# Kernel optimization log

Measured on AMD Instinct MI355X. Metric: run time of the kernel, lower is better.

## Reference

```python
import jax, jax.numpy as jnp
import numpy as np

B, T, C, H = 4, 4096, 1024, 16

def setup_inputs() -> dict:
    key = jax.random.key(0)
    k1, k2, k3, k4 = jax.random.split(key, 4)
    return {
        "x": jax.random.normal(k1, (B, T, C), dtype=jnp.float32),
        "W_attn": jax.random.normal(k2, (C, C), dtype=jnp.float32) * 0.02,
        "b_attn": jnp.zeros((C,), dtype=jnp.float32),
        "W_proj": jax.random.normal(k3, (C, C), dtype=jnp.float32) * 0.02,
        "b_proj": jnp.zeros((C,), dtype=jnp.float32),
        "temp": jnp.ones((H, 1), dtype=jnp.float32),
        "n_head": H,
    }

def reference(x, W_attn, b_attn, W_proj, b_proj, temp, n_head):
    Bb, Tt, Cc = x.shape
    D = Cc // n_head
    # c_attn (torch Linear: x @ W.T + b)
    w = x @ W_attn.T + b_attn                         # (B,T,C)
    w = w.reshape(Bb, Tt, n_head, D).transpose(0, 2, 1, 3)  # (B,H,T,D)
    # F.normalize over token axis (dim=-2), eps=1e-12
    norm = jnp.maximum(jnp.sqrt(jnp.sum(w * w, axis=-2, keepdims=True)), 1e-12)
    w_normed = w / norm
    tmp = jnp.sum(w_normed ** 2, axis=-1) * temp      # (B,H,T) * (H,1) -> (B,H,T)
    Pi = jax.nn.softmax(tmp, axis=1)                  # softmax over heads
    Pi_prob = Pi / (jnp.sum(Pi, axis=-1, keepdims=True) + 1e-8)  # (B,H,T)
    dots = jnp.einsum('bht,bhtd->bhd', Pi_prob, w ** 2)          # (B,H,D)
    attn = 1.0 / (1.0 + dots)                         # (B,H,D)
    y = -(w * Pi[..., None]) * attn[:, :, None, :]    # (B,H,T,D)
    y = y.transpose(0, 2, 1, 3).reshape(Bb, Tt, Cc)
    return y @ W_proj.T + b_proj
```

## Files before the change

kernel.cpp:

```cpp
#include <hip/hip_runtime.h>
#include <hip/hip_bf16.h>

#define BB 4
#define TT 4096
#define CC 1024
#define HH 16
#define DD 64

typedef __attribute__((ext_vector_type(8))) short short8;
typedef __attribute__((ext_vector_type(8))) __bf16 bf16x8;
typedef __attribute__((ext_vector_type(4))) float f32x4;

static __device__ __forceinline__ unsigned short f2bf(float f) {
    unsigned int u = __builtin_bit_cast(unsigned int, f);
    unsigned int r = (u + 0x7FFFu + ((u >> 16) & 1u)) >> 16;
    return (unsigned short)r;
}
static __device__ __forceinline__ float bf2f(unsigned short h) {
    return __builtin_bit_cast(float, ((unsigned int)h) << 16);
}
static __device__ __forceinline__ bf16x8 cvt8(f32x4 a, f32x4 b) {
    bf16x8 r;
    r[0] = (__bf16)a[0]; r[1] = (__bf16)a[1]; r[2] = (__bf16)a[2]; r[3] = (__bf16)a[3];
    r[4] = (__bf16)b[0]; r[5] = (__bf16)b[1]; r[6] = (__bf16)b[2]; r[7] = (__bf16)b[3];
    return r;
}

__global__ void k_f32_to_bf16(const float* __restrict__ src,
                              unsigned short* __restrict__ dst, int n4) {
    int i = blockIdx.x * 256 + threadIdx.x;
    if (i >= n4) return;
    float4 v = ((const float4*)src)[i];
    ushort4 o;
    o.x = f2bf(v.x); o.y = f2bf(v.y); o.z = f2bf(v.z); o.w = f2bf(v.w);
    ((ushort4*)dst)[i] = o;
}

#define GBM 256
#define GBN 256
#define GBK 32

static __device__ __forceinline__ void stage_b16(
    const unsigned short* __restrict__ Gbase, unsigned short* lbase,
    int k0, int K, int wave, int lane)
{
    #pragma unroll
    for (int q = 0; q < 2; ++q) {
        int c = (wave * 2 + q) * 64 + lane;
        int r = c >> 2;
        int j = c & 3;
        int srcj = (j - (r >> 1)) & 3;
        const unsigned short* g = Gbase + (size_t)r * K + k0 + srcj * 8;
        __builtin_amdgcn_global_load_lds(
            (const __attribute__((address_space(1))) void*)g,
            (__attribute__((address_space(3))) void*)(lbase + (wave * 2 + q) * 512),
            16, 0, 0);
    }
}

static __device__ __forceinline__ void stage_a_f32(
    const float* __restrict__ Gbase, float* lbase,
    int k0, int K, int wave, int lane)
{
    #pragma unroll
    for (int q = 0; q < 4; ++q) {
        int c = (wave * 4 + q) * 64 + lane;
        int r = c >> 3;
        int s = c & 7;
        int srcs = s ^ (r & 7);
        const float* g = Gbase + (size_t)r * K + k0 + srcs * 4;
        __builtin_amdgcn_global_load_lds(
            (const __attribute__((address_space(1))) void*)g,
            (__attribute__((address_space(3))) void*)(lbase + (wave * 4 + q) * 256),
            16, 0, 0);
    }
}

template<int MODE>
__global__ __launch_bounds__(512, 2)
void k_gemm256(const void* __restrict__ Asrc,
               const unsigned short* __restrict__ Bsrc,
               const float* __restrict__ bias,
               void* __restrict__ Cout,
               float* __restrict__ S,
               int M, int N, int K)
{
    __shared__ unsigned int Au[3][(MODE == 0) ? 8192 : 4096];
    __shared__ unsigned short Bl[3][8192];
    const int tid  = threadIdx.x;
    const int wave = tid >> 6;
    const int lane = tid & 63;
    const int wr = wave >> 2, wc = wave & 3;
    const int fr = lane & 15, hi = lane >> 4;

    const int wg  = blockIdx.x;
    const int swz = (wg & 7) * 32 + (wg >> 3);
    const int bn  = swz & 3;
    const int bm  = swz >> 2;
    const int nt  = K / GBK;

    const float* Afg = (const float*)Asrc + (size_t)(bm * GBM) * K;
    const unsigned short* Abg = (const unsigned short*)Asrc + (size_t)(bm * GBM) * K;
    const unsigned short* Bbase = Bsrc + (size_t)(bn * GBN) * K;

    f32x4 acc[8][4] = {};

    if (MODE == 0) stage_a_f32(Afg, (float*)Au[0], 0, K, wave, lane);
    else           stage_b16(Abg, (unsigned short*)Au[0], 0, K, wave, lane);
    stage_b16(Bbase, Bl[0], 0, K, wave, lane);
    if (MODE == 0) stage_a_f32(Afg, (float*)Au[1], GBK, K, wave, lane);
    else           stage_b16(Abg, (unsigned short*)Au[1], GBK, K, wave, lane);
    stage_b16(Bbase, Bl[1], GBK, K, wave, lane);
    if (MODE == 0) { asm volatile("s_waitcnt vmcnt(6)" ::: "memory"); }
    else           { asm volatile("s_waitcnt vmcnt(4)" ::: "memory"); }
    __builtin_amdgcn_s_barrier();

    const int sl    = (hi + (fr >> 1)) & 3;
    const int boff  = (wc * 64 + fr) * 32 + sl * 8;
    const int aoffB = (wr * 128 + fr) * 32 + sl * 8;
    const int sw0   = ((2 * hi)     ^ (fr & 7)) * 4;
    const int sw1   = ((2 * hi + 1) ^ (fr & 7)) * 4;
    const int arow  = (wr * 128 + fr) * 32;

    int rb = 0;
    for (int kt = 0; kt < nt; ++kt) {
        const int wb = (rb == 0) ? 2 : rb - 1;
        int ks = kt + 2; if (ks >= nt) ks = nt - 1;
        const unsigned short* Bc = Bl[rb];

        bf16x8 af0[4]; short8 bfr[4];
        if (MODE == 0) {
            const float* Af = (const float*)Au[rb];
            #pragma unroll
            for (int mi = 0; mi < 4; ++mi) {
                f32x4 lo = *(const f32x4*)&Af[arow + mi * 512 + sw0];
                f32x4 h4 = *(const f32x4*)&Af[arow + mi * 512 + sw1];
                af0[mi] = cvt8(lo, h4);
            }
        } else {
            const unsigned short* Ab = (const unsigned short*)Au[rb];
            #pragma unroll
            for (int mi = 0; mi < 4; ++mi)
                af0[mi] = __builtin_bit_cast(bf16x8, *(const short8*)&Ab[aoffB + mi * 512]);
        }
        #pragma unroll
        for (int ni = 0; ni < 4; ++ni)
            bfr[ni] = *(const short8*)&Bc[boff + ni * 512];
        if (MODE == 0) stage_a_f32(Afg, (float*)Au[wb], ks * GBK, K, wave, lane);
        else           stage_b16(Abg, (unsigned short*)Au[wb], ks * GBK, K, wave, lane);
        stage_b16(Bbase, Bl[wb], ks * GBK, K, wave, lane);
        __builtin_amdgcn_s_barrier();
        __builtin_amdgcn_s_setprio(1);
        #pragma unroll
        for (int mi = 0; mi < 4; ++mi)
            #pragma unroll
            for (int ni = 0; ni < 4; ++ni)
                acc[mi][ni] = __builtin_amdgcn_mfma_f32_16x16x32_bf16(
                    af0[mi], __builtin_bit_cast(bf16x8, bfr[ni]), acc[mi][ni], 0, 0, 0);
        __builtin_amdgcn_s_setprio(0);
        __builtin_amdgcn_s_barrier();

        bf16x8 af1[4];
        if (MODE == 0) {
            const float* Af = (const float*)Au[rb];
            #pragma unroll
            for (int mi = 0; mi < 4; ++mi) {
                f32x4 lo = *(const f32x4*)&Af[arow + (4 + mi) * 512 + sw0];
                f32x4 h4 = *(const f32x4*)&Af[arow + (4 + mi) * 512 + sw1];
                af1[mi] = cvt8(lo, h4);
            }
        } else {
            const unsigned short* Ab = (const unsigned short*)Au[rb];
            #pragma unroll
            for (int mi = 0; mi < 4; ++mi)
                af1[mi] = __builtin_bit_cast(bf16x8, *(const short8*)&Ab[aoffB + (4 + mi) * 512]);
        }
        if (MODE == 0) { asm volatile("s_waitcnt vmcnt(6)" ::: "memory"); }
        else           { asm volatile("s_waitcnt vmcnt(4)" ::: "memory"); }
        __builtin_amdgcn_s_barrier();
        __builtin_amdgcn_s_setprio(1);
        #pragma unroll
        for (int mi = 0; mi < 4; ++mi)
            #pragma unroll
            for (int ni = 0; ni < 4; ++ni)
                acc[4 + mi][ni] = __builtin_amdgcn_mfma_f32_16x16x32_bf16(
                    af1[mi], __builtin_bit_cast(bf16x8, bfr[ni]), acc[4 + mi][ni], 0, 0, 0);
        __builtin_amdgcn_s_setprio(0);
        __builtin_amdgcn_s_barrier();

        rb = (rb == 2) ? 0 : rb + 1;
    }

    __syncthreads();

    const int cg = fr;
    const int rg = hi * 4;
    float* sblk = (float*)&Bl[0][0];
    if (MODE == 0) {
        if (tid < GBN) sblk[tid] = 0.f;
        __syncthreads();
    }
    float csum[4] = {};
    #pragma unroll
    for (int mi = 0; mi < 8; ++mi) {
        #pragma unroll
        for (int ni = 0; ni < 4; ++ni) {
            int col = bn * GBN + wc * 64 + ni * 16 + cg;
            float bv = bias[col];
            #pragma unroll
            for (int j = 0; j < 4; ++j) {
                int row = bm * GBM + wr * 128 + mi * 16 + rg + j;
                float v = acc[mi][ni][j] + bv;
                if (MODE == 0) {
                    ((unsigned short*)Cout)[(size_t)row * N + col] = f2bf(v);
                    csum[ni] += v * v;
                } else {
                    ((float*)Cout)[(size_t)row * N + col] = v;
                }
            }
        }
    }
    if (MODE == 0) {
        #pragma unroll
        for (int ni = 0; ni < 4; ++ni)
            atomicAdd(&sblk[wc * 64 + ni * 16 + cg], csum[ni]);
        __syncthreads();
        const int b = bm >> 4;
        if (tid < GBN) atomicAdd(&S[b * CC + bn * GBN + tid], sblk[tid]);
    }
}

__global__ __launch_bounds__(256)
void k_row_softmax(const unsigned short* __restrict__ w16, const float* __restrict__ S,
                   const float* __restrict__ temp,
                   float* __restrict__ Pi, float* __restrict__ dotsU,
                   float* __restrict__ sumPi)
{
    __shared__ float dots_local[CC];
    __shared__ float sPi_local[HH];
    const int tid  = threadIdx.x;
    const int wave = tid >> 6;
    const int lane = tid & 63;
    const int bb   = blockIdx.x >> 7;
    const int tile = blockIdx.x & 127;

    for (int c = tid; c < CC; c += 256) dots_local[c] = 0.f;
    if (tid < HH) sPi_local[tid] = 0.f;
    __syncthreads();

    const int g3 = lane >> 3;
    const int li = lane & 7;

    float inv[2][8], tsc[2];
    #pragma unroll
    for (int q = 0; q < 2; ++q) {
        int c = q * 512 + lane * 8;
        const float4* sp = (const float4*)&S[bb * CC + c];
        float4 s0 = sp[0], s1 = sp[1];
        inv[q][0] = 1.f / fmaxf(s0.x, 1e-24f); inv[q][1] = 1.f / fmaxf(s0.y, 1e-24f);
        inv[q][2] = 1.f / fmaxf(s0.z, 1e-24f); inv[q][3] = 1.f / fmaxf(s0.w, 1e-24f);
        inv[q][4] = 1.f / fmaxf(s1.x, 1e-24f); inv[q][5] = 1.f / fmaxf(s1.y, 1e-24f);
        inv[q][6] = 1.f / fmaxf(s1.z, 1e-24f); inv[q][7] = 1.f / fmaxf(s1.w, 1e-24f);
        tsc[q] = temp[q * 8 + g3];
    }

    float dacc[2][8] = {};
    float sPiAcc[2] = {};

    for (int i = 0; i < 8; ++i) {
        int t = tile * 32 + wave * 8 + i;
        const unsigned short* row = w16 + ((size_t)bb * TT + t) * CC;
        float wf[2][8];
        float pq[2];
        #pragma unroll
        for (int q = 0; q < 2; ++q) {
            short8 v = *(const short8*)&row[q * 512 + lane * 8];
            float s = 0.f;
            #pragma unroll
            for (int j = 0; j < 8; ++j) {
                wf[q][j] = bf2f((unsigned short)v[j]);
                s += wf[q][j] * wf[q][j] * inv[q][j];
            }
            pq[q] = s;
        }
        #pragma unroll
        for (int off = 1; off < 8; off <<= 1) {
            pq[0] += __shfl_xor(pq[0], off);
            pq[1] += __shfl_xor(pq[1], off);
        }
        pq[0] *= tsc[0]; pq[1] *= tsc[1];
        float mx = fmaxf(pq[0], pq[1]);
        mx = fmaxf(mx, __shfl_xor(mx, 8));
        mx = fmaxf(mx, __shfl_xor(mx, 16));
        mx = fmaxf(mx, __shfl_xor(mx, 32));
        float e0 = __expf(pq[0] - mx), e1 = __expf(pq[1] - mx);
        float ss = e0 + e1;
        ss += __shfl_xor(ss, 8);
        ss += __shfl_xor(ss, 16);
        ss += __shfl_xor(ss, 32);
        float rs = 1.f / ss;
        float piv[2] = { e0 * rs, e1 * rs };
        #pragma unroll
        for (int q = 0; q < 2; ++q) {
            #pragma unroll
            for (int j = 0; j < 8; ++j)
                dacc[q][j] += piv[q] * wf[q][j] * wf[q][j];
            if (li == 0) {
                Pi[((size_t)(bb * HH + q * 8 + g3)) * TT + t] = piv[q];
                sPiAcc[q] += piv[q];
            }
        }
    }

    #pragma unroll
    for (int q = 0; q < 2; ++q) {
        int c = q * 512 + lane * 8;
        #pragma unroll
        for (int j = 0; j < 8; ++j)
            atomicAdd(&dots_local[c + j], dacc[q][j]);
        if (li == 0) atomicAdd(&sPi_local[q * 8 + g3], sPiAcc[q]);
    }
    __syncthreads();
    for (int c = tid; c < CC; c += 256) atomicAdd(&dotsU[bb * CC + c], dots_local[c]);
    if (tid < HH) atomicAdd(&sumPi[bb * HH + tid], sPi_local[tid]);
}

__global__ void k_attnscale(const float* __restrict__ dotsU,
                            const float* __restrict__ sumPi,
                            float* __restrict__ attnScale) {
    int i = blockIdx.x * 256 + threadIdx.x;
    if (i >= BB * CC) return;
    int b = i >> 10;
    int h = (i >> 6) & 15;
    float sp = sumPi[b * HH + h] + 1e-8f;
    attnScale[i] = 1.f / (1.f + dotsU[i] / sp);
}

__global__ void k_make_y(unsigned short* __restrict__ wy, const float* __restrict__ Pi,
                         const float* __restrict__ attnScale)
{
    size_t i = (size_t)blockIdx.x * 256 + threadIdx.x;
    size_t flat = i * 8;
    int c = (int)(flat & (CC - 1));
    size_t bt = flat >> 10;
    int t = (int)(bt & (TT - 1));
    int b = (int)(bt >> 12);
    int h = c >> 6;
    float pi = Pi[((size_t)(b * HH + h)) * TT + t];
    short8 wv = *(const short8*)&wy[flat];
    f32x4 a0 = *(const f32x4*)&attnScale[b * CC + c];
    f32x4 a1 = *(const f32x4*)&attnScale[b * CC + c + 4];
    short8 o;
    #pragma unroll
    for (int j = 0; j < 4; ++j) {
        o[j]     = (short)f2bf(-(bf2f((unsigned short)wv[j])     * pi) * a0[j]);
        o[4 + j] = (short)f2bf(-(bf2f((unsigned short)wv[4 + j]) * pi) * a1[j]);
    }
    *(short8*)&wy[flat] = o;
}

extern "C" void kernel_launch(void* const* d_in, const int* in_sizes, int n_in,
                              void* d_out, int out_size, void* d_ws, size_t ws_size,
                              hipStream_t stream) {
    const float* x      = (const float*)d_in[0];
    const float* W_attn = (const float*)d_in[1];
    const float* b_attn = (const float*)d_in[2];
    const float* W_proj = (const float*)d_in[3];
    const float* b_proj = (const float*)d_in[4];
    const float* temp   = (const float*)d_in[5];

    char* ws = (char*)d_ws;
    unsigned short* w16  = (unsigned short*)(ws);
    unsigned short* Wa16 = (unsigned short*)(ws + 33554432);
    unsigned short* Wp16 = (unsigned short*)(ws + 35651584);
    float* Pi        = (float*)(ws + 37748736);
    float* S         = (float*)(ws + 38797312);
    float* dotsU     = (float*)(ws + 38813696);
    float* sumPi     = (float*)(ws + 38830080);
    float* attnScale = (float*)(ws + 38830336);

    k_f32_to_bf16<<<dim3(1024), dim3(256), 0, stream>>>(W_attn, Wa16, 262144);
    k_f32_to_bf16<<<dim3(1024), dim3(256), 0, stream>>>(W_proj, Wp16, 262144);

    hipMemsetAsync(S, 0, 16384 + 16384 + 256, stream);

    k_gemm256<0><<<dim3(256), dim3(512), 0, stream>>>(
        x, Wa16, b_attn, w16, S, BB * TT, CC, CC);

    k_row_softmax<<<dim3(512), dim3(256), 0, stream>>>(w16, S, temp, Pi, dotsU, sumPi);

    k_attnscale<<<dim3(16), dim3(256), 0, stream>>>(dotsU, sumPi, attnScale);

    k_make_y<<<dim3(8192), dim3(256), 0, stream>>>(w16, Pi, attnScale);

    k_gemm256<1><<<dim3(256), dim3(512), 0, stream>>>(
        w16, Wp16, b_proj, d_out, nullptr, BB * TT, CC, CC);
}
```

Before: 150.6 us.

## Pre-convert x to bf16 and use a 4-stage unified LDS pipeline in GEMM

Adds a separate kernel that converts x from fp32 to bf16 into the output buffer as scratch, so the first GEMM loads bf16 A tiles instead of fp32 tiles that it converted in registers. The GEMM is reworked to use a single 4-deep LDS ring holding both A and B tiles, with prefetch three steps ahead. The A and B stages are split across the two half-iterations, and B fragments are reloaded in each half. This removes the per-iteration fp32 LDS traffic and conversion work, at the cost of an extra pass over x in global memory and more LDS per block.

```diff
diff --git a/kernel.cpp b/kernel.cpp
--- a/kernel.cpp
+++ b/kernel.cpp
@@ -18,12 +18,6 @@
 }
 static __device__ __forceinline__ float bf2f(unsigned short h) {
     return __builtin_bit_cast(float, ((unsigned int)h) << 16);
-}
-static __device__ __forceinline__ bf16x8 cvt8(f32x4 a, f32x4 b) {
-    bf16x8 r;
-    r[0] = (__bf16)a[0]; r[1] = (__bf16)a[1]; r[2] = (__bf16)a[2]; r[3] = (__bf16)a[3];
-    r[4] = (__bf16)b[0]; r[5] = (__bf16)b[1]; r[6] = (__bf16)b[2]; r[7] = (__bf16)b[3];
-    return r;
 }
 
 __global__ void k_f32_to_bf16(const float* __restrict__ src,
@@ -40,7 +34,7 @@
 #define GBN 256
 #define GBK 32
 
-static __device__ __forceinline__ void stage_b16(
+static __device__ __forceinline__ void stage_tile32(
     const unsigned short* __restrict__ Gbase, unsigned short* lbase,
     int k0, int K, int wave, int lane)
 {
@@ -58,144 +52,101 @@
     }
 }
 
-static __device__ __forceinline__ void stage_a_f32(
-    const float* __restrict__ Gbase, float* lbase,
-    int k0, int K, int wave, int lane)
-{
-    #pragma unroll
-    for (int q = 0; q < 4; ++q) {
-        int c = (wave * 4 + q) * 64 + lane;
-        int r = c >> 3;
-        int s = c & 7;
-        int srcs = s ^ (r & 7);
-        const float* g = Gbase + (size_t)r * K + k0 + srcs * 4;
-        __builtin_amdgcn_global_load_lds(
-            (const __attribute__((address_space(1))) void*)g,
-            (__attribute__((address_space(3))) void*)(lbase + (wave * 4 + q) * 256),
-            16, 0, 0);
-    }
-}
-
 template<int MODE>
 __global__ __launch_bounds__(512, 2)
-void k_gemm256(const void* __restrict__ Asrc,
-               const unsigned short* __restrict__ Bsrc,
+void k_gemm256(const unsigned short* __restrict__ A,
+               const unsigned short* __restrict__ B,
                const float* __restrict__ bias,
                void* __restrict__ Cout,
                float* __restrict__ S,
                int M, int N, int K)
 {
-    __shared__ unsigned int Au[3][(MODE == 0) ? 8192 : 4096];
-    __shared__ unsigned short Bl[3][8192];
+    __shared__ unsigned short lds[4][16384];
     const int tid  = threadIdx.x;
     const int wave = tid >> 6;
     const int lane = tid & 63;
-    const int wr = wave >> 2, wc = wave & 3;
-    const int fr = lane & 15, hi = lane >> 4;
+    const int wr = wave >> 2;
+    const int wc = wave & 3;
+    const int fr = lane & 15;
+    const int hi = lane >> 4;
 
     const int wg  = blockIdx.x;
     const int swz = (wg & 7) * 32 + (wg >> 3);
     const int bn  = swz & 3;
     const int bm  = swz >> 2;
-    const int nt  = K / GBK;
-
-    const float* Afg = (const float*)Asrc + (size_t)(bm * GBM) * K;
-    const unsigned short* Abg = (const unsigned short*)Asrc + (size_t)(bm * GBM) * K;
-    const unsigned short* Bbase = Bsrc + (size_t)(bn * GBN) * K;
+
+    const unsigned short* Abase = A + (size_t)(bm * GBM) * K;
+    const unsigned short* Bbase = B + (size_t)(bn * GBN) * K;
+
+    const int nt = K / GBK;
+
+    const int sl   = (hi + (fr >> 1)) & 3;
+    const int aoff = (wr * 128 + fr) * 32 + sl * 8;
+    const int boff = 8192 + (wc * 64 + fr) * 32 + sl * 8;
 
     f32x4 acc[8][4] = {};
 
-    if (MODE == 0) stage_a_f32(Afg, (float*)Au[0], 0, K, wave, lane);
-    else           stage_b16(Abg, (unsigned short*)Au[0], 0, K, wave, lane);
-    stage_b16(Bbase, Bl[0], 0, K, wave, lane);
-    if (MODE == 0) stage_a_f32(Afg, (float*)Au[1], GBK, K, wave, lane);
-    else           stage_b16(Abg, (unsigned short*)Au[1], GBK, K, wave, lane);
-    stage_b16(Bbase, Bl[1], GBK, K, wave, lane);
-    if (MODE == 0) { asm volatile("s_waitcnt vmcnt(6)" ::: "memory"); }
-    else           { asm volatile("s_waitcnt vmcnt(4)" ::: "memory"); }
+    stage_tile32(Abase, lds[0],        0,       K, wave, lane);
+    stage_tile32(Bbase, lds[0] + 8192, 0,       K, wave, lane);
+    stage_tile32(Abase, lds[1],        GBK,     K, wave, lane);
+    stage_tile32(Bbase, lds[1] + 8192, GBK,     K, wave, lane);
+    stage_tile32(Abase, lds[2],        2 * GBK, K, wave, lane);
+    stage_tile32(Bbase, lds[2] + 8192, 2 * GBK, K, wave, lane);
+    asm volatile("s_waitcnt vmcnt(8)" ::: "memory");
     __builtin_amdgcn_s_barrier();
 
-    const int sl    = (hi + (fr >> 1)) & 3;
-    const int boff  = (wc * 64 + fr) * 32 + sl * 8;
-    const int aoffB = (wr * 128 + fr) * 32 + sl * 8;
-    const int sw0   = ((2 * hi)     ^ (fr & 7)) * 4;
-    const int sw1   = ((2 * hi + 1) ^ (fr & 7)) * 4;
-    const int arow  = (wr * 128 + fr) * 32;
-
-    int rb = 0;
     for (int kt = 0; kt < nt; ++kt) {
-        const int wb = (rb == 0) ? 2 : rb - 1;
-        int ks = kt + 2; if (ks >= nt) ks = nt - 1;
-        const unsigned short* Bc = Bl[rb];
-
-        bf16x8 af0[4]; short8 bfr[4];
-        if (MODE == 0) {
-            const float* Af = (const float*)Au[rb];
-            #pragma unroll
-            for (int mi = 0; mi < 4; ++mi) {
-                f32x4 lo = *(const f32x4*)&Af[arow + mi * 512 + sw0];
-                f32x4 h4 = *(const f32x4*)&Af[arow + mi * 512 + sw1];
-                af0[mi] = cvt8(lo, h4);
-            }
-        } else {
-            const unsigned short* Ab = (const unsigned short*)Au[rb];
-            #pragma unroll
-            for (int mi = 0; mi < 4; ++mi)
-                af0[mi] = __builtin_bit_cast(bf16x8, *(const short8*)&Ab[aoffB + mi * 512]);
-        }
-        #pragma unroll
-        for (int ni = 0; ni < 4; ++ni)
-            bfr[ni] = *(const short8*)&Bc[boff + ni * 512];
-        if (MODE == 0) stage_a_f32(Afg, (float*)Au[wb], ks * GBK, K, wave, lane);
-        else           stage_b16(Abg, (unsigned short*)Au[wb], ks * GBK, K, wave, lane);
-        stage_b16(Bbase, Bl[wb], ks * GBK, K, wave, lane);
+        const unsigned short* buf = lds[kt & 3];
+        unsigned short* sbuf = lds[(kt + 3) & 3];
+        int k3 = kt + 3; if (k3 >= nt) k3 = nt - 1;
+
+        short8 af0[4], bf0[4];
+        #pragma unroll
+        for (int i = 0; i < 4; ++i) af0[i] = *(const short8*)&buf[aoff + i * 512];
+        #pragma unroll
+        for (int i = 0; i < 4; ++i) bf0[i] = *(const short8*)&buf[boff + i * 512];
+        stage_tile32(Abase, sbuf, k3 * GBK, K, wave, lane);
         __builtin_amdgcn_s_barrier();
+        asm volatile("s_waitcnt lgkmcnt(0)" ::: "memory");
         __builtin_amdgcn_s_setprio(1);
         #pragma unroll
         for (int mi = 0; mi < 4; ++mi)
             #pragma unroll
             for (int ni = 0; ni < 4; ++ni)
                 acc[mi][ni] = __builtin_amdgcn_mfma_f32_16x16x32_bf16(
-                    af0[mi], __builtin_bit_cast(bf16x8, bfr[ni]), acc[mi][ni], 0, 0, 0);
+                    __builtin_bit_cast(bf16x8, af0[mi]),
+                    __builtin_bit_cast(bf16x8, bf0[ni]),
+                    acc[mi][ni], 0, 0, 0);
         __builtin_amdgcn_s_setprio(0);
         __builtin_amdgcn_s_barrier();
 
-        bf16x8 af1[4];
-        if (MODE == 0) {
-            const float* Af = (const float*)Au[rb];
-            #pragma unroll
-            for (int mi = 0; mi < 4; ++mi) {
-                f32x4 lo = *(const f32x4*)&Af[arow + (4 + mi) * 512 + sw0];
-                f32x4 h4 = *(const f32x4*)&Af[arow + (4 + mi) * 512 + sw1];
-                af1[mi] = cvt8(lo, h4);
-            }
-        } else {
-            const unsigned short* Ab = (const unsigned short*)Au[rb];
-            #pragma unroll
-            for (int mi = 0; mi < 4; ++mi)
-                af1[mi] = __builtin_bit_cast(bf16x8, *(const short8*)&Ab[aoffB + (4 + mi) * 512]);
-        }
-        if (MODE == 0) { asm volatile("s_waitcnt vmcnt(6)" ::: "memory"); }
-        else           { asm volatile("s_waitcnt vmcnt(4)" ::: "memory"); }
+        short8 af1[4], bf1[4];
+        #pragma unroll
+        for (int i = 0; i < 4; ++i) af1[i] = *(const short8*)&buf[aoff + (4 + i) * 512];
+        #pragma unroll
+        for (int i = 0; i < 4; ++i) bf1[i] = *(const short8*)&buf[boff + i * 512];
+        stage_tile32(Bbase, sbuf + 8192, k3 * GBK, K, wave, lane);
+        asm volatile("s_waitcnt vmcnt(8)" ::: "memory");
         __builtin_amdgcn_s_barrier();
+        asm volatile("s_waitcnt lgkmcnt(0)" ::: "memory");
         __builtin_amdgcn_s_setprio(1);
         #pragma unroll
         for (int mi = 0; mi < 4; ++mi)
             #pragma unroll
             for (int ni = 0; ni < 4; ++ni)
                 acc[4 + mi][ni] = __builtin_amdgcn_mfma_f32_16x16x32_bf16(
-                    af1[mi], __builtin_bit_cast(bf16x8, bfr[ni]), acc[4 + mi][ni], 0, 0, 0);
+                    __builtin_bit_cast(bf16x8, af1[mi]),
+                    __builtin_bit_cast(bf16x8, bf1[ni]),
+                    acc[4 + mi][ni], 0, 0, 0);
         __builtin_amdgcn_s_setprio(0);
         __builtin_amdgcn_s_barrier();
-
-        rb = (rb == 2) ? 0 : rb + 1;
     }
 
     __syncthreads();
 
     const int cg = fr;
     const int rg = hi * 4;
-    float* sblk = (float*)&Bl[0][0];
+    float* sblk = (float*)&lds[0][0];
     if (MODE == 0) {
         if (tid < GBN) sblk[tid] = 0.f;
         __syncthreads();
@@ -369,6 +320,8 @@
     const float* b_proj = (const float*)d_in[4];
     const float* temp   = (const float*)d_in[5];
 
+    unsigned short* xb = (unsigned short*)d_out;
+
     char* ws = (char*)d_ws;
     unsigned short* w16  = (unsigned short*)(ws);
     unsigned short* Wa16 = (unsigned short*)(ws + 33554432);
@@ -379,13 +332,14 @@
     float* sumPi     = (float*)(ws + 38830080);
     float* attnScale = (float*)(ws + 38830336);
 
+    k_f32_to_bf16<<<dim3(16384), dim3(256), 0, stream>>>(x, xb, 4194304);
     k_f32_to_bf16<<<dim3(1024), dim3(256), 0, stream>>>(W_attn, Wa16, 262144);
     k_f32_to_bf16<<<dim3(1024), dim3(256), 0, stream>>>(W_proj, Wp16, 262144);
 
     hipMemsetAsync(S, 0, 16384 + 16384 + 256, stream);
 
     k_gemm256<0><<<dim3(256), dim3(512), 0, stream>>>(
-        x, Wa16, b_attn, w16, S, BB * TT, CC, CC);
+        xb, Wa16, b_attn, w16, S, BB * TT, CC, CC);
 
     k_row_softmax<<<dim3(512), dim3(256), 0, stream>>>(w16, S, temp, Pi, dotsU, sumPi);
 
```

Result: faster. 142.8 us (-5.2%).
